# Performance work log

Hardware: AMD Instinct MI355X
Metric: run time of the kernel (lower is better)

The kernel has to match this reference:

```python
import jax, jax.numpy as jnp
import numpy as np

N, E = 50000, 200000
SIZES = [16, 32, 16]
EDIM = 8
EPS = 1e-5


def setup_inputs() -> dict:
    key = jax.random.key(0)
    ks = jax.random.split(key, 16)
    inp = {
        "x": jax.random.normal(ks[0], (N, SIZES[0]), jnp.float32),
        "edge_attr": jax.random.normal(ks[1], (E, EDIM), jnp.float32),
        "edge_index": jax.random.randint(ks[2], (2, E), 0, N, dtype=jnp.int32),
    }
    ki = 3
    for l in range(2):
        fin, fout = SIZES[l], SIZES[l + 1]
        m = fin * fout
        # xavier-ish init matching torch.nn.init.xavier_uniform_ scales
        inp[f"W1_{l}"] = jax.random.normal(ks[ki], (EDIM, m), jnp.float32) / np.float32(np.sqrt(EDIM)); ki += 1
        inp[f"b1_{l}"] = jnp.zeros((m,), jnp.float32)
        inp[f"W2_{l}"] = jax.random.normal(ks[ki], (m, m), jnp.float32) * np.float32(0.01 / np.sqrt(m)); ki += 1
        inp[f"b2_{l}"] = jnp.zeros((m,), jnp.float32)
        inp[f"root_{l}"] = jax.random.normal(ks[ki], (fin, fout), jnp.float32) / np.float32(np.sqrt(fin)); ki += 1
        inp[f"bias_{l}"] = jnp.zeros((fout,), jnp.float32)
        inp[f"gamma_{l}"] = jnp.ones((fout,), jnp.float32)
        inp[f"beta_{l}"] = jnp.zeros((fout,), jnp.float32)
    return inp


def _lrelu(v):
    return jnp.where(v >= 0, v, 0.01 * v)


def _nnconv(x, src, dst, edge_attr, W1, b1, W2, b2, root, bias, fin, fout):
    # edge MLP -> per-edge weight matrix [E, fin, fout]
    h = _lrelu(edge_attr @ W1 + b1) @ W2 + b2
    h = h.reshape(-1, fin, fout)
    # gather source node features, tiny per-edge matmul
    msg = jnp.einsum('ei,eio->eo', x[src], h)  # [E, fout]
    # scatter-mean aggregate at destination nodes
    agg = jax.ops.segment_sum(msg, dst, num_segments=N)
    deg = jax.ops.segment_sum(jnp.ones((msg.shape[0],), msg.dtype), dst, num_segments=N)
    agg = agg / jnp.maximum(deg, 1.0)[:, None]
    return agg + x @ root + bias


def _bn(v, gamma, beta):
    # BatchNorm1d (training mode: batch stats, biased variance)
    mu = v.mean(0)
    var = v.var(0)
    return (v - mu) * jax.lax.rsqrt(var + EPS) * gamma + beta


def reference(x, edge_attr,
              W1_0, b1_0, W2_0, b2_0, root_0, bias_0, gamma_0, beta_0,
              W1_1, b1_1, W2_1, b2_1, root_1, bias_1, gamma_1, beta_1,
              edge_index):
    src, dst = edge_index[0], edge_index[1]
    h = _nnconv(x, src, dst, edge_attr, W1_0, b1_0, W2_0, b2_0, root_0, bias_0, SIZES[0], SIZES[1])
    h = _lrelu(_bn(h, gamma_0, beta_0))
    h = _nnconv(h, src, dst, edge_attr, W1_1, b1_1, W2_1, b2_1, root_1, bias_1, SIZES[1], SIZES[2])
    return _bn(h, gamma_1, beta_1)
```

## Files before the change

kernel.cpp:

```cpp
#include <hip/hip_runtime.h>
#include <hip/hip_bf16.h>

typedef __attribute__((ext_vector_type(4))) float f32x4;
typedef __attribute__((ext_vector_type(8))) short s16x8;
typedef __attribute__((ext_vector_type(4))) int int4v;

#define DEVI __device__ __forceinline__

constexpr int NN = 50000;
constexpr int NE = 200000;
constexpr float BN_EPS = 1e-5f;

DEVI float bfbits2f(unsigned v) { union { unsigned u; float f; } t; t.u = v << 16; return t.f; }
DEVI float lrelu_f(float v) { return v >= 0.f ? v : 0.01f * v; }

__global__ void k_transpose_w2(const float* __restrict__ A0, const float* __restrict__ A1,
                               __hip_bfloat16* __restrict__ T0, __hip_bfloat16* __restrict__ T1) {
  const float* W2 = blockIdx.y ? A1 : A0;
  __hip_bfloat16* W2T = blockIdx.y ? T1 : T0;
  __shared__ float tile[32][33];
  int bx = blockIdx.x % 16, by = blockIdx.x / 16;
  int t = threadIdx.x;
  int r = t / 32, c = t % 32;
  for (int rr = r; rr < 32; rr += 8)
    tile[rr][c] = W2[(size_t)(by * 32 + rr) * 512 + bx * 32 + c];
  __syncthreads();
  for (int rr = r; rr < 32; rr += 8)
    W2T[(size_t)(bx * 32 + rr) * 512 + by * 32 + c] = __float2bfloat16(tile[c][rr]);
}

__global__ void k_transpose_w1(const float* __restrict__ A0, const float* __restrict__ A1,
                               __hip_bfloat16* __restrict__ T0, __hip_bfloat16* __restrict__ T1) {
  const float* W1 = blockIdx.y ? A1 : A0;
  __hip_bfloat16* W1T = blockIdx.y ? T1 : T0;
  int tid = blockIdx.x * 256 + threadIdx.x;
  if (tid < 8 * 512) {
    int k = tid / 512, n = tid % 512;
    W1T[n * 8 + k] = __float2bfloat16(W1[tid]);
  }
}

__global__ void k_count(const int* __restrict__ dst, int* __restrict__ cnt) {
  int e = blockIdx.x * 256 + threadIdx.x;
  if (e < NE) atomicAdd(&cnt[dst[e]], 1);
}

constexpr int SCAN_ELEMS = 1024;
__global__ void k_scan1(const int* __restrict__ cnt, int* __restrict__ base, int* __restrict__ aux, int n) {
  __shared__ int sw[256];
  int b = blockIdx.x, t = threadIdx.x;
  int i0 = b * SCAN_ELEMS + t * 4;
  int v[4]; int s = 0;
  #pragma unroll
  for (int j = 0; j < 4; j++) { int idx = i0 + j; v[j] = (idx < n) ? cnt[idx] : 0; s += v[j]; }
  sw[t] = s; __syncthreads();
  for (int d = 1; d < 256; d <<= 1) {
    int val = (t >= d) ? sw[t - d] : 0;
    __syncthreads();
    sw[t] += val;
    __syncthreads();
  }
  int run = (t > 0) ? sw[t - 1] : 0;
  #pragma unroll
  for (int j = 0; j < 4; j++) { int idx = i0 + j; if (idx < n) base[idx] = run; run += v[j]; }
  if (t == 255) aux[b] = sw[255];
}

__global__ void k_scan2(int* aux, int nb) {
  if (threadIdx.x == 0 && blockIdx.x == 0) {
    int run = 0;
    for (int i = 0; i < nb; i++) { int v = aux[i]; aux[i] = run; run += v; }
  }
}

__global__ void k_scan3(int* __restrict__ base, int* __restrict__ cursor, const int* __restrict__ aux, int n) {
  int i = blockIdx.x * 256 + threadIdx.x;
  if (i < n) { int v = base[i] + aux[i / SCAN_ELEMS]; base[i] = v; cursor[i] = v; }
}

__global__ void k_place(const int* __restrict__ dst, int* __restrict__ cursor, int* __restrict__ perm) {
  int e = blockIdx.x * 256 + threadIdx.x;
  if (e < NE) { int p = atomicAdd(&cursor[dst[e]], 1); perm[p] = e; }
}

template <int FIN, int FOUT>
__global__ __launch_bounds__(512, 2)
void k_edge(const float* __restrict__ x, const float* __restrict__ ea,
            const int* __restrict__ srcI,
            const __hip_bfloat16* __restrict__ W1T, const float* __restrict__ b1,
            const __hip_bfloat16* __restrict__ W2T, const float* __restrict__ b2,
            __hip_bfloat16* __restrict__ msgb)
{
  static_assert(FOUT == 32 || FOUT == 16, "");
  constexpr int TM = 512;
  constexpr int CG = 32;
  constexpr int NCGI = 16;
  constexpr int KH = 256;
  constexpr int NKC = 4;
  constexpr int NOT = FOUT / 16;
  constexpr int BSTRIDE = KH * 2 + 16;
  constexpr int XLDS = TM + 8;

  __shared__ __align__(16) char ubuf[2 * CG * BSTRIDE];
  __shared__ __align__(16) __hip_bfloat16 xlt[FIN][XLDS];

  const int tid = threadIdx.x;
  const int lane = tid & 63, w = tid >> 6;
  const int l15 = lane & 15, l4 = lane >> 4;
  const int e0 = blockIdx.x * TM;
  const int rem = min(TM, NE - e0);
  const int wrow0 = w * 64;

  s16x8 afe[4];
  {
    int er = e0 + min(tid, rem - 1);
    float4 v0 = *(const float4*)(ea + (size_t)er * 8);
    float4 v1 = *(const float4*)(ea + (size_t)er * 8 + 4);
    union { s16x8 v; int i4[4]; } earow;
    __hip_bfloat16* p = (__hip_bfloat16*)&earow;
    p[0] = __float2bfloat16(v0.x); p[1] = __float2bfloat16(v0.y);
    p[2] = __float2bfloat16(v0.z); p[3] = __float2bfloat16(v0.w);
    p[4] = __float2bfloat16(v1.x); p[5] = __float2bfloat16(v1.y);
    p[6] = __float2bfloat16(v1.z); p[7] = __float2bfloat16(v1.w);
    #pragma unroll
    for (int rt = 0; rt < 4; rt++) {
      union { s16x8 v; int i4[4]; } t2;
      #pragma unroll
      for (int q = 0; q < 4; q++) t2.i4[q] = __shfl(earow.i4[q], rt * 16 + l15);
      afe[rt] = (lane < 16) ? t2.v : (s16x8)0;
    }
    int s = srcI[er];
    #pragma unroll
    for (int q = 0; q < FIN / 4; q++) {
      float4 xv4 = *(const float4*)(x + (size_t)s * FIN + q * 4);
      xlt[q * 4 + 0][tid] = __float2bfloat16(xv4.x);
      xlt[q * 4 + 1][tid] = __float2bfloat16(xv4.y);
      xlt[q * 4 + 2][tid] = __float2bfloat16(xv4.z);
      xlt[q * 4 + 3][tid] = __float2bfloat16(xv4.w);
    }
  }

  f32x4 msg[4][NOT];
  #pragma unroll
  for (int rt = 0; rt < 4; rt++)
    #pragma unroll
    for (int ot = 0; ot < NOT; ot++) msg[rt][ot] = (f32x4)(0.f);

  s16x8 af[NKC][4][2];
  int4v sr0, sr1;

  for (int sw = 0; sw < 2; ++sw) {
    {
      int n = tid >> 4, s0 = tid & 15;
      const char* gp = (const char*)(W2T + (size_t)n * 512 + sw * KH);
      sr0 = *(const int4v*)(gp + s0 * 16);
      sr1 = *(const int4v*)(gp + (s0 + 16) * 16);
    }
    char* gme = ubuf + w * 4096;
    #pragma unroll
    for (int h = 0; h < 2; ++h) {
      #pragma unroll
      for (int kc = 0; kc < NKC; kc++) {
        #pragma unroll
        for (int ct = 0; ct < 4; ct++) {
          int c = sw * KH + kc * 64 + ct * 16 + l15;
          s16x8 bw = *(const s16x8*)(W1T + c * 8);
          bw = (lane < 16) ? bw : (s16x8)0;
          float b1v = b1[c];
          #pragma unroll
          for (int rt2 = 0; rt2 < 2; rt2++) {
            f32x4 d = __builtin_amdgcn_mfma_f32_16x16x32_bf16(afe[h * 2 + rt2], bw, (f32x4)(0.f), 0, 0, 0);
            #pragma unroll
            for (int r = 0; r < 4; r++) {
              int rloc = rt2 * 16 + l4 * 4 + r;
              float gv = d[r] + b1v;
              gv = gv >= 0.f ? gv : 0.01f * gv;
              int byt = (rloc * 128 + (ct * 16 + l15) * 2) ^ (((rloc + (rloc >> 2)) & 3) << 5);
              *(__hip_bfloat16*)(gme + byt) = __float2bfloat16(gv);
            }
          }
        }
        #pragma unroll
        for (int rt2 = 0; rt2 < 2; rt2++)
          #pragma unroll
          for (int ks = 0; ks < 2; ks++) {
            int rloc = rt2 * 16 + l15;
            int byt = (rloc * 128 + (ks * 32 + l4 * 8) * 2) ^ (((rloc + (rloc >> 2)) & 3) << 5);
            af[kc][h * 2 + rt2][ks] = *(const s16x8*)(gme + byt);
          }
      }
    }
    #pragma unroll
    for (int kc = 0; kc < NKC; kc++)
      #pragma unroll
      for (int rt = 0; rt < 4; rt++)
        #pragma unroll
        for (int ks = 0; ks < 2; ks++)
          asm volatile("" : "+v"(af[kc][rt][ks]));
    __syncthreads();
    {
      int n = tid >> 4, s0 = tid & 15;
      *(int4v*)(ubuf + n * BSTRIDE + s0 * 16) = sr0;
      *(int4v*)(ubuf + n * BSTRIDE + (s0 + 16) * 16) = sr1;
    }
    __syncthreads();

    for (int cgi = 0; cgi < NCGI; ++cgi) {
      if (cgi + 1 < NCGI) {
        int n = tid >> 4, s0 = tid & 15;
        const char* gp = (const char*)(W2T + (size_t)((cgi + 1) * CG + n) * 512 + sw * KH);
        sr0 = *(const int4v*)(gp + s0 * 16);
        sr1 = *(const int4v*)(gp + (s0 + 16) * 16);
      }
      const char* bb = ubuf + (cgi & 1) * (CG * BSTRIDE);
      f32x4 acc[4][2];
      #pragma unroll
      for (int rt = 0; rt < 4; rt++) { acc[rt][0] = (f32x4)(0.f); acc[rt][1] = (f32x4)(0.f); }

      #pragma unroll
      for (int kc = 0; kc < NKC; kc++)
        #pragma unroll
        for (int ct = 0; ct < 2; ct++) {
          int c = ct * 16 + l15;
          #pragma unroll
          for (int ks = 0; ks < 2; ks++) {
            const s16x8 bw = *(const s16x8*)(bb + c * BSTRIDE + kc * 128 + ks * 64 + l4 * 16);
            #pragma unroll
            for (int rt = 0; rt < 4; rt++)
              acc[rt][ct] = __builtin_amdgcn_mfma_f32_16x16x32_bf16(af[kc][rt][ks], bw, acc[rt][ct], 0, 0, 0);
          }
        }

      #pragma unroll
      for (int ct = 0; ct < 2; ct++) {
        float b2v = (sw == 0) ? b2[cgi * CG + ct * 16 + l15] : 0.f;
        const int iv = (FOUT == 32) ? cgi : (cgi * 2 + ct);
        const int ot = (FOUT == 32) ? ct : 0;
        #pragma unroll
        for (int rt = 0; rt < 4; rt++) {
          int rbase = wrow0 + rt * 16 + l4 * 4;
          ushort4 xv = *(const ushort4*)(&xlt[iv][rbase]);
          msg[rt][ot][0] += bfbits2f(xv.x) * (acc[rt][ct][0] + b2v);
          msg[rt][ot][1] += bfbits2f(xv.y) * (acc[rt][ct][1] + b2v);
          msg[rt][ot][2] += bfbits2f(xv.z) * (acc[rt][ct][2] + b2v);
          msg[rt][ot][3] += bfbits2f(xv.w) * (acc[rt][ct][3] + b2v);
        }
      }
      if (cgi + 1 < NCGI) {
        int n = tid >> 4, s0 = tid & 15;
        char* bw2 = ubuf + ((cgi + 1) & 1) * (CG * BSTRIDE);
        *(int4v*)(bw2 + n * BSTRIDE + s0 * 16) = sr0;
        *(int4v*)(bw2 + n * BSTRIDE + (s0 + 16) * 16) = sr1;
      }
      __syncthreads();
    }
  }

  #pragma unroll
  for (int rt = 0; rt < 4; rt++)
    #pragma unroll
    for (int r = 0; r < 4; r++) {
      int row = wrow0 + rt * 16 + l4 * 4 + r;
      if (row < rem) {
        #pragma unroll
        for (int ot = 0; ot < NOT; ot++)
          msgb[(size_t)(e0 + row) * FOUT + ot * 16 + l15] = __float2bfloat16(msg[rt][ot][r]);
      }
    }
}

template <int FIN, int FOUT>
__global__ void k_node_agg(const __hip_bfloat16* __restrict__ msgb, const int* __restrict__ perm,
                           const int* __restrict__ base,
                           const float* __restrict__ x,
                           const float* __restrict__ root,
                           const float* __restrict__ bias,
                           float* __restrict__ h)
{
  __shared__ float rl[FIN * FOUT];
  constexpr int NPB = 256 / FOUT;
  int t = threadIdx.x;
  for (int i = t; i < FIN * FOUT; i += 256) rl[i] = root[i];
  __syncthreads();
  int n = blockIdx.x * NPB + t / FOUT;
  int o = t % FOUT;
  if (n >= NN) return;
  int s = base[n];
  int e = (n + 1 < NN) ? base[n + 1] : NE;
  float sum = 0.f;
  for (int j = s; j < e; j++)
    sum += __bfloat162float(msgb[(size_t)perm[j] * FOUT + o]);
  float acc = sum / fmaxf((float)(e - s), 1.f) + bias[o];
  #pragma unroll
  for (int i = 0; i < FIN; i++)
    acc += x[(size_t)n * FIN + i] * rl[i * FOUT + o];
  h[(size_t)n * FOUT + o] = acc;
}

template <int FOUT>
__global__ void k_stats(const float* __restrict__ h, float* __restrict__ ssum, float* __restrict__ ssq) {
  constexpr int RPB = 256 / FOUT;
  int t = threadIdx.x;
  int o = t % FOUT, rr = t / FOUT;
  float v = 0.f, v2 = 0.f;
  for (int r = blockIdx.x * RPB + rr; r < NN; r += gridDim.x * RPB) {
    float y = h[(size_t)r * FOUT + o];
    v += y; v2 += y * y;
  }
  #pragma unroll
  for (int d = FOUT; d < 64; d <<= 1) { v += __shfl_xor(v, d); v2 += __shfl_xor(v2, d); }
  __shared__ float sv[4][32], sq[4][32];
  int wv = t >> 6, ln = t & 63;
  if (ln < FOUT) { sv[wv][ln] = v; sq[wv][ln] = v2; }
  __syncthreads();
  if (t < FOUT) {
    float a = 0.f, b = 0.f;
    #pragma unroll
    for (int w2 = 0; w2 < 4; w2++) { a += sv[w2][t]; b += sq[w2][t]; }
    atomicAdd(&ssum[t], a);
    atomicAdd(&ssq[t], b);
  }
}

template <int FOUT, bool LRELU>
__global__ void k_bn(const float* __restrict__ h, const float* __restrict__ ssum,
                     const float* __restrict__ ssq, const float* __restrict__ gamma,
                     const float* __restrict__ beta, float* __restrict__ out)
{
  int idx = blockIdx.x * 256 + threadIdx.x;
  if (idx * 4 >= NN * FOUT) return;
  float4 v = *(const float4*)(h + (size_t)idx * 4);
  float r[4] = {v.x, v.y, v.z, v.w};
  #pragma unroll
  for (int j = 0; j < 4; j++) {
    int o = (idx * 4 + j) % FOUT;
    float mu = ssum[o] * (1.f / NN);
    float var = ssq[o] * (1.f / NN) - mu * mu;
    float sc = rsqrtf(var + BN_EPS) * gamma[o];
    float y = (r[j] - mu) * sc + beta[o];
    if (LRELU) y = lrelu_f(y);
    r[j] = y;
  }
  *(float4*)(out + (size_t)idx * 4) = make_float4(r[0], r[1], r[2], r[3]);
}

extern "C" void kernel_launch(void* const* d_in, const int* in_sizes, int n_in,
                              void* d_out, int out_size, void* d_ws, size_t ws_size,
                              hipStream_t stream)
{
  const float* x0    = (const float*)d_in[0];
  const float* ea    = (const float*)d_in[1];
  const int*   ei    = (const int*)d_in[2];
  const float* W1_0  = (const float*)d_in[3];
  const float* b1_0  = (const float*)d_in[4];
  const float* W2_0  = (const float*)d_in[5];
  const float* b2_0  = (const float*)d_in[6];
  const float* root0 = (const float*)d_in[7];
  const float* bias0 = (const float*)d_in[8];
  const float* gam0  = (const float*)d_in[9];
  const float* bet0  = (const float*)d_in[10];
  const float* W1_1  = (const float*)d_in[11];
  const float* b1_1  = (const float*)d_in[12];
  const float* W2_1  = (const float*)d_in[13];
  const float* b2_1  = (const float*)d_in[14];
  const float* root1 = (const float*)d_in[15];
  const float* bias1 = (const float*)d_in[16];
  const float* gam1  = (const float*)d_in[17];
  const float* bet1  = (const float*)d_in[18];
  const int* srcI = ei;
  const int* dstI = ei + NE;

  char* ws = (char*)d_ws;
  size_t off = 0;
  auto alloc = [&](size_t bytes) { char* p = ws + off; off += (bytes + 255) & ~(size_t)255; return p; };
  int*   cnt   = (int*)alloc(50048 * 4);
  float* ssum0 = (float*)alloc(32 * 4);
  float* ssq0  = (float*)alloc(32 * 4);
  float* ssum1 = (float*)alloc(16 * 4);
  float* ssq1  = (float*)alloc(16 * 4);
  size_t zero_bytes = off;
  int*   base   = (int*)alloc(50048 * 4);
  int*   cursor = (int*)alloc(50048 * 4);
  int*   aux    = (int*)alloc(64 * 4);
  int*   perm   = (int*)alloc((size_t)NE * 4);
  __hip_bfloat16* msgb = (__hip_bfloat16*)alloc((size_t)NE * 32 * 2);
  float* h0 = (float*)alloc((size_t)NN * 32 * 4);
  float* h1 = (float*)alloc((size_t)NN * 16 * 4);
  float* x1 = (float*)alloc((size_t)NN * 32 * 4);
  __hip_bfloat16* W2T0 = (__hip_bfloat16*)alloc(512 * 512 * 2);
  __hip_bfloat16* W2T1 = (__hip_bfloat16*)alloc(512 * 512 * 2);
  __hip_bfloat16* W1T0 = (__hip_bfloat16*)alloc(512 * 8 * 2);
  __hip_bfloat16* W1T1 = (__hip_bfloat16*)alloc(512 * 8 * 2);

  hipMemsetAsync(d_ws, 0, zero_bytes, stream);

  k_transpose_w2<<<dim3(256, 2), 256, 0, stream>>>(W2_0, W2_1, W2T0, W2T1);
  k_transpose_w1<<<dim3(16, 2), 256, 0, stream>>>(W1_0, W1_1, W1T0, W1T1);

  constexpr int NSB = (NN + SCAN_ELEMS - 1) / SCAN_ELEMS;
  k_count<<<(NE + 255) / 256, 256, 0, stream>>>(dstI, cnt);
  k_scan1<<<NSB, 256, 0, stream>>>(cnt, base, aux, NN);
  k_scan2<<<1, 64, 0, stream>>>(aux, NSB);
  k_scan3<<<(NN + 255) / 256, 256, 0, stream>>>(base, cursor, aux, NN);
  k_place<<<(NE + 255) / 256, 256, 0, stream>>>(dstI, cursor, perm);

  constexpr int TM = 512;
  k_edge<16, 32><<<(NE + TM - 1) / TM, 512, 0, stream>>>(x0, ea, srcI, W1T0, b1_0, W2T0, b2_0, msgb);
  k_node_agg<16, 32><<<(NN + 7) / 8, 256, 0, stream>>>(msgb, perm, base, x0, root0, bias0, h0);
  k_stats<32><<<128, 256, 0, stream>>>(h0, ssum0, ssq0);
  k_bn<32, true><<<((NN * 32 / 4) + 255) / 256, 256, 0, stream>>>(h0, ssum0, ssq0, gam0, bet0, x1);

  k_edge<32, 16><<<(NE + TM - 1) / TM, 512, 0, stream>>>(x1, ea, srcI, W1T1, b1_1, W2T1, b2_1, msgb);
  k_node_agg<32, 16><<<(NN + 15) / 16, 256, 0, stream>>>(msgb, perm, base, x1, root1, bias1, h1);
  k_stats<16><<<128, 256, 0, stream>>>(h1, ssum1, ssq1);
  k_bn<16, false><<<((NN * 16 / 4) + 255) / 256, 256, 0, stream>>>(h1, ssum1, ssq1, gam1, bet1, (float*)d_out);
}
```

Measured before the change: 389.6 us.

## Split edge-MLP K dimension into four passes to raise occupancy

The fused edge kernel now processes the hidden dimension in four 128-wide K slices instead of two 256-wide ones. This halves the register-resident A fragments so launch bounds can request 4 waves per SIMD instead of 2, and it shrinks the LDS staging buffers. It also caches b1/b2 in shared memory. The cost is recomputing the first-layer MFMA and shuffles twice as often and running twice as many W2 streaming loops and barriers.

```diff
diff --git a/kernel.cpp b/kernel.cpp
--- a/kernel.cpp
+++ b/kernel.cpp
@@ -84,7 +84,7 @@
 }
 
 template <int FIN, int FOUT>
-__global__ __launch_bounds__(512, 2)
+__global__ __launch_bounds__(512, 4)
 void k_edge(const float* __restrict__ x, const float* __restrict__ ea,
             const int* __restrict__ srcI,
             const __hip_bfloat16* __restrict__ W1T, const float* __restrict__ b1,
@@ -95,14 +95,17 @@
   constexpr int TM = 512;
   constexpr int CG = 32;
   constexpr int NCGI = 16;
-  constexpr int KH = 256;
-  constexpr int NKC = 4;
+  constexpr int KH = 128;
+  constexpr int NSW = 4;
+  constexpr int NKS = 4;
   constexpr int NOT = FOUT / 16;
-  constexpr int BSTRIDE = KH * 2 + 16;
+  constexpr int BSTRIDE = 272;
   constexpr int XLDS = TM + 8;
 
-  __shared__ __align__(16) char ubuf[2 * CG * BSTRIDE];
+  __shared__ __align__(16) char ubuf[32768];
   __shared__ __align__(16) __hip_bfloat16 xlt[FIN][XLDS];
+  __shared__ float b1l[512];
+  __shared__ float b2l[512];
 
   const int tid = threadIdx.x;
   const int lane = tid & 63, w = tid >> 6;
@@ -111,24 +114,18 @@
   const int rem = min(TM, NE - e0);
   const int wrow0 = w * 64;
 
-  s16x8 afe[4];
+  b1l[tid] = b1[tid];
+  b2l[tid] = b2[tid];
+  union { s16x8 v; int i4[4]; } earow;
   {
     int er = e0 + min(tid, rem - 1);
     float4 v0 = *(const float4*)(ea + (size_t)er * 8);
     float4 v1 = *(const float4*)(ea + (size_t)er * 8 + 4);
-    union { s16x8 v; int i4[4]; } earow;
     __hip_bfloat16* p = (__hip_bfloat16*)&earow;
     p[0] = __float2bfloat16(v0.x); p[1] = __float2bfloat16(v0.y);
     p[2] = __float2bfloat16(v0.z); p[3] = __float2bfloat16(v0.w);
     p[4] = __float2bfloat16(v1.x); p[5] = __float2bfloat16(v1.y);
     p[6] = __float2bfloat16(v1.z); p[7] = __float2bfloat16(v1.w);
-    #pragma unroll
-    for (int rt = 0; rt < 4; rt++) {
-      union { s16x8 v; int i4[4]; } t2;
-      #pragma unroll
-      for (int q = 0; q < 4; q++) t2.i4[q] = __shfl(earow.i4[q], rt * 16 + l15);
-      afe[rt] = (lane < 16) ? t2.v : (s16x8)0;
-    }
     int s = srcI[er];
     #pragma unroll
     for (int q = 0; q < FIN / 4; q++) {
@@ -139,6 +136,7 @@
       xlt[q * 4 + 3][tid] = __float2bfloat16(xv4.w);
     }
   }
+  __syncthreads();
 
   f32x4 msg[4][NOT];
   #pragma unroll
@@ -146,112 +144,92 @@
     #pragma unroll
     for (int ot = 0; ot < NOT; ot++) msg[rt][ot] = (f32x4)(0.f);
 
-  s16x8 af[NKC][4][2];
-  int4v sr0, sr1;
-
-  for (int sw = 0; sw < 2; ++sw) {
-    {
-      int n = tid >> 4, s0 = tid & 15;
-      const char* gp = (const char*)(W2T + (size_t)n * 512 + sw * KH);
-      sr0 = *(const int4v*)(gp + s0 * 16);
-      sr1 = *(const int4v*)(gp + (s0 + 16) * 16);
+  s16x8 af[NKS][4];
+  const int st_n = tid >> 4, st_s = tid & 15;
+  const char* W2Tb = (const char*)W2T;
+
+  for (int sw = 0; sw < NSW; ++sw) {
+    s16x8 afe[4];
+    #pragma unroll
+    for (int rt = 0; rt < 4; rt++) {
+      union { s16x8 v; int i4[4]; } t2;
+      #pragma unroll
+      for (int q = 0; q < 4; q++) t2.i4[q] = __shfl(earow.i4[q], rt * 16 + l15);
+      afe[rt] = (lane < 16) ? t2.v : (s16x8)0;
     }
     char* gme = ubuf + w * 4096;
     #pragma unroll
-    for (int h = 0; h < 2; ++h) {
-      #pragma unroll
-      for (int kc = 0; kc < NKC; kc++) {
+    for (int kst = 0; kst < NKS; ++kst) {
+      #pragma unroll
+      for (int ct = 0; ct < 2; ++ct) {
+        int c = sw * KH + kst * 32 + ct * 16 + l15;
+        s16x8 bw = *(const s16x8*)(W1T + c * 8);
+        bw = (lane < 16) ? bw : (s16x8)0;
+        float b1v = b1l[c];
         #pragma unroll
-        for (int ct = 0; ct < 4; ct++) {
-          int c = sw * KH + kc * 64 + ct * 16 + l15;
-          s16x8 bw = *(const s16x8*)(W1T + c * 8);
-          bw = (lane < 16) ? bw : (s16x8)0;
-          float b1v = b1[c];
+        for (int rt = 0; rt < 4; rt++) {
+          f32x4 d = __builtin_amdgcn_mfma_f32_16x16x32_bf16(afe[rt], bw, (f32x4)(0.f), 0, 0, 0);
           #pragma unroll
-          for (int rt2 = 0; rt2 < 2; rt2++) {
-            f32x4 d = __builtin_amdgcn_mfma_f32_16x16x32_bf16(afe[h * 2 + rt2], bw, (f32x4)(0.f), 0, 0, 0);
-            #pragma unroll
-            for (int r = 0; r < 4; r++) {
-              int rloc = rt2 * 16 + l4 * 4 + r;
-              float gv = d[r] + b1v;
-              gv = gv >= 0.f ? gv : 0.01f * gv;
-              int byt = (rloc * 128 + (ct * 16 + l15) * 2) ^ (((rloc + (rloc >> 2)) & 3) << 5);
-              *(__hip_bfloat16*)(gme + byt) = __float2bfloat16(gv);
-            }
+          for (int r = 0; r < 4; r++) {
+            int rloc = rt * 16 + l4 * 4 + r;
+            float gv = d[r] + b1v;
+            gv = gv >= 0.f ? gv : 0.01f * gv;
+            int byt = (rloc * 64 + (ct * 16 + l15) * 2) ^ (((rloc >> 2) & 3) << 4);
+            *(__hip_bfloat16*)(gme + byt) = __float2bfloat16(gv);
           }
         }
+      }
+      #pragma unroll
+      for (int rt = 0; rt < 4; rt++) {
+        int rloc2 = rt * 16 + l15;
+        int byt = (rloc2 * 64 + l4 * 16) ^ (((rloc2 >> 2) & 3) << 4);
+        af[kst][rt] = *(const s16x8*)(gme + byt);
+      }
+    }
+    #pragma unroll
+    for (int kst = 0; kst < NKS; kst++)
+      #pragma unroll
+      for (int rt = 0; rt < 4; rt++)
+        asm volatile("" : "+v"(af[kst][rt]));
+
+    int4v sr = *(const int4v*)(W2Tb + (size_t)st_n * 1024 + sw * 256 + st_s * 16);
+    __syncthreads();
+    *(int4v*)(ubuf + st_n * BSTRIDE + st_s * 16) = sr;
+    __syncthreads();
+
+    for (int cgi = 0; cgi < NCGI; ++cgi) {
+      if (cgi + 1 < NCGI)
+        sr = *(const int4v*)(W2Tb + (size_t)((cgi + 1) * CG + st_n) * 1024 + sw * 256 + st_s * 16);
+      const char* bb = ubuf + (cgi & 1) * (CG * BSTRIDE);
+      const int rdbase = l15 * BSTRIDE + l4 * 16;
+
+      #pragma unroll
+      for (int ct = 0; ct < 2; ++ct) {
+        f32x4 acc[4];
+        acc[0] = (f32x4)(0.f); acc[1] = (f32x4)(0.f);
+        acc[2] = (f32x4)(0.f); acc[3] = (f32x4)(0.f);
         #pragma unroll
-        for (int rt2 = 0; rt2 < 2; rt2++)
+        for (int kst = 0; kst < NKS; ++kst) {
+          const s16x8 bw = *(const s16x8*)(bb + ct * (16 * BSTRIDE) + rdbase + kst * 64);
           #pragma unroll
-          for (int ks = 0; ks < 2; ks++) {
-            int rloc = rt2 * 16 + l15;
-            int byt = (rloc * 128 + (ks * 32 + l4 * 8) * 2) ^ (((rloc + (rloc >> 2)) & 3) << 5);
-            af[kc][h * 2 + rt2][ks] = *(const s16x8*)(gme + byt);
-          }
-      }
-    }
-    #pragma unroll
-    for (int kc = 0; kc < NKC; kc++)
-      #pragma unroll
-      for (int rt = 0; rt < 4; rt++)
-        #pragma unroll
-        for (int ks = 0; ks < 2; ks++)
-          asm volatile("" : "+v"(af[kc][rt][ks]));
-    __syncthreads();
-    {
-      int n = tid >> 4, s0 = tid & 15;
-      *(int4v*)(ubuf + n * BSTRIDE + s0 * 16) = sr0;
-      *(int4v*)(ubuf + n * BSTRIDE + (s0 + 16) * 16) = sr1;
-    }
-    __syncthreads();
-
-    for (int cgi = 0; cgi < NCGI; ++cgi) {
-      if (cgi + 1 < NCGI) {
-        int n = tid >> 4, s0 = tid & 15;
-        const char* gp = (const char*)(W2T + (size_t)((cgi + 1) * CG + n) * 512 + sw * KH);
-        sr0 = *(const int4v*)(gp + s0 * 16);
-        sr1 = *(const int4v*)(gp + (s0 + 16) * 16);
-      }
-      const char* bb = ubuf + (cgi & 1) * (CG * BSTRIDE);
-      f32x4 acc[4][2];
-      #pragma unroll
-      for (int rt = 0; rt < 4; rt++) { acc[rt][0] = (f32x4)(0.f); acc[rt][1] = (f32x4)(0.f); }
-
-      #pragma unroll
-      for (int kc = 0; kc < NKC; kc++)
-        #pragma unroll
-        for (int ct = 0; ct < 2; ct++) {
-          int c = ct * 16 + l15;
-          #pragma unroll
-          for (int ks = 0; ks < 2; ks++) {
-            const s16x8 bw = *(const s16x8*)(bb + c * BSTRIDE + kc * 128 + ks * 64 + l4 * 16);
-            #pragma unroll
-            for (int rt = 0; rt < 4; rt++)
-              acc[rt][ct] = __builtin_amdgcn_mfma_f32_16x16x32_bf16(af[kc][rt][ks], bw, acc[rt][ct], 0, 0, 0);
-          }
+          for (int rt = 0; rt < 4; rt++)
+            acc[rt] = __builtin_amdgcn_mfma_f32_16x16x32_bf16(af[kst][rt], bw, acc[rt], 0, 0, 0);
         }
-
-      #pragma unroll
-      for (int ct = 0; ct < 2; ct++) {
-        float b2v = (sw == 0) ? b2[cgi * CG + ct * 16 + l15] : 0.f;
+        float b2v = (sw == 0) ? b2l[cgi * CG + ct * 16 + l15] : 0.f;
         const int iv = (FOUT == 32) ? cgi : (cgi * 2 + ct);
         const int ot = (FOUT == 32) ? ct : 0;
         #pragma unroll
         for (int rt = 0; rt < 4; rt++) {
           int rbase = wrow0 + rt * 16 + l4 * 4;
           ushort4 xv = *(const ushort4*)(&xlt[iv][rbase]);
-          msg[rt][ot][0] += bfbits2f(xv.x) * (acc[rt][ct][0] + b2v);
-          msg[rt][ot][1] += bfbits2f(xv.y) * (acc[rt][ct][1] + b2v);
-          msg[rt][ot][2] += bfbits2f(xv.z) * (acc[rt][ct][2] + b2v);
-          msg[rt][ot][3] += bfbits2f(xv.w) * (acc[rt][ct][3] + b2v);
+          msg[rt][ot][0] += bfbits2f(xv.x) * (acc[rt][0] + b2v);
+          msg[rt][ot][1] += bfbits2f(xv.y) * (acc[rt][1] + b2v);
+          msg[rt][ot][2] += bfbits2f(xv.z) * (acc[rt][2] + b2v);
+          msg[rt][ot][3] += bfbits2f(xv.w) * (acc[rt][3] + b2v);
         }
       }
-      if (cgi + 1 < NCGI) {
-        int n = tid >> 4, s0 = tid & 15;
-        char* bw2 = ubuf + ((cgi + 1) & 1) * (CG * BSTRIDE);
-        *(int4v*)(bw2 + n * BSTRIDE + s0 * 16) = sr0;
-        *(int4v*)(bw2 + n * BSTRIDE + (s0 + 16) * 16) = sr1;
-      }
+      if (cgi + 1 < NCGI)
+        *(int4v*)(ubuf + ((cgi + 1) & 1) * (CG * BSTRIDE) + st_n * BSTRIDE + st_s * 16) = sr;
       __syncthreads();
     }
   }
```

Result: slower. 1.098 ms (+181.7%).

## Halve edge-kernel block size, split LDS buffers, XOR-swizzle W2 tile layout

Applied to the files above, without the earlier changes.

The edge kernel now uses 256-thread blocks covering 256 edges instead of 512, which doubles the grid and doubles how many times each block reloads W2. The staging buffer is split into a dedicated per-wave hidden-activation buffer and an unpadded W2 double buffer, and the W2 tile uses an XOR swizzle instead of row padding. This removes the barrier that separated hidden-layer writes from W2 staging and is meant to reduce LDS bank conflicts. The edge-attribute shuffle is recomputed inside each sweep. The trade-off is more total W2 traffic from global memory in exchange for better occupancy and fewer stalls.

```diff
diff --git a/kernel.cpp b/kernel.cpp
--- a/kernel.cpp
+++ b/kernel.cpp
@@ -84,7 +84,7 @@
 }
 
 template <int FIN, int FOUT>
-__global__ __launch_bounds__(512, 2)
+__global__ __launch_bounds__(256, 2)
 void k_edge(const float* __restrict__ x, const float* __restrict__ ea,
             const int* __restrict__ srcI,
             const __hip_bfloat16* __restrict__ W1T, const float* __restrict__ b1,
@@ -92,16 +92,16 @@
             __hip_bfloat16* __restrict__ msgb)
 {
   static_assert(FOUT == 32 || FOUT == 16, "");
-  constexpr int TM = 512;
+  constexpr int TM = 256;
   constexpr int CG = 32;
   constexpr int NCGI = 16;
   constexpr int KH = 256;
   constexpr int NKC = 4;
   constexpr int NOT = FOUT / 16;
-  constexpr int BSTRIDE = KH * 2 + 16;
   constexpr int XLDS = TM + 8;
 
-  __shared__ __align__(16) char ubuf[2 * CG * BSTRIDE];
+  __shared__ __align__(16) char bbuf[2][CG * 512];
+  __shared__ __align__(16) char gbuf[4][4096];
   __shared__ __align__(16) __hip_bfloat16 xlt[FIN][XLDS];
 
   const int tid = threadIdx.x;
@@ -111,24 +111,16 @@
   const int rem = min(TM, NE - e0);
   const int wrow0 = w * 64;
 
-  s16x8 afe[4];
+  union { s16x8 v; int i4[4]; } earow;
   {
     int er = e0 + min(tid, rem - 1);
     float4 v0 = *(const float4*)(ea + (size_t)er * 8);
     float4 v1 = *(const float4*)(ea + (size_t)er * 8 + 4);
-    union { s16x8 v; int i4[4]; } earow;
     __hip_bfloat16* p = (__hip_bfloat16*)&earow;
     p[0] = __float2bfloat16(v0.x); p[1] = __float2bfloat16(v0.y);
     p[2] = __float2bfloat16(v0.z); p[3] = __float2bfloat16(v0.w);
     p[4] = __float2bfloat16(v1.x); p[5] = __float2bfloat16(v1.y);
     p[6] = __float2bfloat16(v1.z); p[7] = __float2bfloat16(v1.w);
-    #pragma unroll
-    for (int rt = 0; rt < 4; rt++) {
-      union { s16x8 v; int i4[4]; } t2;
-      #pragma unroll
-      for (int q = 0; q < 4; q++) t2.i4[q] = __shfl(earow.i4[q], rt * 16 + l15);
-      afe[rt] = (lane < 16) ? t2.v : (s16x8)0;
-    }
     int s = srcI[er];
     #pragma unroll
     for (int q = 0; q < FIN / 4; q++) {
@@ -147,16 +139,25 @@
     for (int ot = 0; ot < NOT; ot++) msg[rt][ot] = (f32x4)(0.f);
 
   s16x8 af[NKC][4][2];
-  int4v sr0, sr1;
+  const int st_col = tid >> 3, st_s = tid & 7;
+  const char* W2Tb = (const char*)W2T;
+  char* gme = gbuf[w];
+  int4v sr[4];
 
   for (int sw = 0; sw < 2; ++sw) {
     {
-      int n = tid >> 4, s0 = tid & 15;
-      const char* gp = (const char*)(W2T + (size_t)n * 512 + sw * KH);
-      sr0 = *(const int4v*)(gp + s0 * 16);
-      sr1 = *(const int4v*)(gp + (s0 + 16) * 16);
-    }
-    char* gme = ubuf + w * 4096;
+      const char* gp = W2Tb + (size_t)st_col * 1024 + sw * 512;
+      #pragma unroll
+      for (int j = 0; j < 4; j++) sr[j] = *(const int4v*)(gp + st_s * 16 + j * 128);
+    }
+    s16x8 afe[4];
+    #pragma unroll
+    for (int rt = 0; rt < 4; rt++) {
+      union { s16x8 v; int i4[4]; } t2;
+      #pragma unroll
+      for (int q = 0; q < 4; q++) t2.i4[q] = __shfl(earow.i4[q], rt * 16 + l15);
+      afe[rt] = (lane < 16) ? t2.v : (s16x8)0;
+    }
     #pragma unroll
     for (int h = 0; h < 2; ++h) {
       #pragma unroll
@@ -175,7 +176,7 @@
               int rloc = rt2 * 16 + l4 * 4 + r;
               float gv = d[r] + b1v;
               gv = gv >= 0.f ? gv : 0.01f * gv;
-              int byt = (rloc * 128 + (ct * 16 + l15) * 2) ^ (((rloc + (rloc >> 2)) & 3) << 5);
+              int byt = (rloc * 128 + (ct * 16 + l15) * 2) ^ ((rloc & 7) << 4);
               *(__hip_bfloat16*)(gme + byt) = __float2bfloat16(gv);
             }
           }
@@ -185,7 +186,7 @@
           #pragma unroll
           for (int ks = 0; ks < 2; ks++) {
             int rloc = rt2 * 16 + l15;
-            int byt = (rloc * 128 + (ks * 32 + l4 * 8) * 2) ^ (((rloc + (rloc >> 2)) & 3) << 5);
+            int byt = (rloc * 128 + (ks * 32 + l4 * 8) * 2) ^ ((rloc & 7) << 4);
             af[kc][h * 2 + rt2][ks] = *(const s16x8*)(gme + byt);
           }
       }
@@ -197,22 +198,19 @@
         #pragma unroll
         for (int ks = 0; ks < 2; ks++)
           asm volatile("" : "+v"(af[kc][rt][ks]));
-    __syncthreads();
-    {
-      int n = tid >> 4, s0 = tid & 15;
-      *(int4v*)(ubuf + n * BSTRIDE + s0 * 16) = sr0;
-      *(int4v*)(ubuf + n * BSTRIDE + (s0 + 16) * 16) = sr1;
-    }
+
+    #pragma unroll
+    for (int j = 0; j < 4; j++)
+      *(int4v*)(&bbuf[0][st_col * 512 + (((st_s + 8 * j) ^ (st_col & 7)) << 4)]) = sr[j];
     __syncthreads();
 
     for (int cgi = 0; cgi < NCGI; ++cgi) {
       if (cgi + 1 < NCGI) {
-        int n = tid >> 4, s0 = tid & 15;
-        const char* gp = (const char*)(W2T + (size_t)((cgi + 1) * CG + n) * 512 + sw * KH);
-        sr0 = *(const int4v*)(gp + s0 * 16);
-        sr1 = *(const int4v*)(gp + (s0 + 16) * 16);
+        const char* gp = W2Tb + (size_t)((cgi + 1) * CG + st_col) * 1024 + sw * 512;
+        #pragma unroll
+        for (int j = 0; j < 4; j++) sr[j] = *(const int4v*)(gp + st_s * 16 + j * 128);
       }
-      const char* bb = ubuf + (cgi & 1) * (CG * BSTRIDE);
+      const char* bb = bbuf[cgi & 1];
       f32x4 acc[4][2];
       #pragma unroll
       for (int rt = 0; rt < 4; rt++) { acc[rt][0] = (f32x4)(0.f); acc[rt][1] = (f32x4)(0.f); }
@@ -221,10 +219,11 @@
       for (int kc = 0; kc < NKC; kc++)
         #pragma unroll
         for (int ct = 0; ct < 2; ct++) {
-          int c = ct * 16 + l15;
+          const int c = ct * 16 + l15;
           #pragma unroll
           for (int ks = 0; ks < 2; ks++) {
-            const s16x8 bw = *(const s16x8*)(bb + c * BSTRIDE + kc * 128 + ks * 64 + l4 * 16);
+            const int slot = kc * 8 + ks * 4 + l4;
+            const s16x8 bw = *(const s16x8*)(bb + c * 512 + ((slot ^ (c & 7)) << 4));
             #pragma unroll
             for (int rt = 0; rt < 4; rt++)
               acc[rt][ct] = __builtin_amdgcn_mfma_f32_16x16x32_bf16(af[kc][rt][ks], bw, acc[rt][ct], 0, 0, 0);
@@ -247,10 +246,10 @@
         }
       }
       if (cgi + 1 < NCGI) {
-        int n = tid >> 4, s0 = tid & 15;
-        char* bw2 = ubuf + ((cgi + 1) & 1) * (CG * BSTRIDE);
-        *(int4v*)(bw2 + n * BSTRIDE + s0 * 16) = sr0;
-        *(int4v*)(bw2 + n * BSTRIDE + (s0 + 16) * 16) = sr1;
+        char* bw2 = bbuf[(cgi + 1) & 1];
+        #pragma unroll
+        for (int j = 0; j < 4; j++)
+          *(int4v*)(&bw2[st_col * 512 + (((st_s + 8 * j) ^ (st_col & 7)) << 4)]) = sr[j];
       }
       __syncthreads();
     }
@@ -404,13 +403,13 @@
   k_scan3<<<(NN + 255) / 256, 256, 0, stream>>>(base, cursor, aux, NN);
   k_place<<<(NE + 255) / 256, 256, 0, stream>>>(dstI, cursor, perm);
 
-  constexpr int TM = 512;
-  k_edge<16, 32><<<(NE + TM - 1) / TM, 512, 0, stream>>>(x0, ea, srcI, W1T0, b1_0, W2T0, b2_0, msgb);
+  constexpr int TM = 256;
+  k_edge<16, 32><<<(NE + TM - 1) / TM, 256, 0, stream>>>(x0, ea, srcI, W1T0, b1_0, W2T0, b2_0, msgb);
   k_node_agg<16, 32><<<(NN + 7) / 8, 256, 0, stream>>>(msgb, perm, base, x0, root0, bias0, h0);
   k_stats<32><<<128, 256, 0, stream>>>(h0, ssum0, ssq0);
   k_bn<32, true><<<((NN * 32 / 4) + 255) / 256, 256, 0, stream>>>(h0, ssum0, ssq0, gam0, bet0, x1);
 
-  k_edge<32, 16><<<(NE + TM - 1) / TM, 512, 0, stream>>>(x1, ea, srcI, W1T1, b1_1, W2T1, b2_1, msgb);
+  k_edge<32, 16><<<(NE + TM - 1) / TM, 256, 0, stream>>>(x1, ea, srcI, W1T1, b1_1, W2T1, b2_1, msgb);
   k_node_agg<32, 16><<<(NN + 15) / 16, 256, 0, stream>>>(msgb, perm, base, x1, root1, bias1, h1);
   k_stats<16><<<128, 256, 0, stream>>>(h1, ssum1, ssq1);
   k_bn<16, false><<<((NN * 16 / 4) + 255) / 256, 256, 0, stream>>>(h1, ssum1, ssq1, gam1, bet1, (float*)d_out);
```

After: 392.5 us. About the same (+0.7%).
